# Performance work log

Measured on AMD Instinct MI355X. Metric: run time of the kernel, lower is better.

The kernel has to match this reference:

```python
import jax, jax.numpy as jnp
import numpy as np

B, IN, H = 131072, 128, 128


def _linear_params(key, out_dim, in_dim):
    k1, k2 = jax.random.split(key)
    bound = 1.0 / np.sqrt(in_dim)
    W = jax.random.uniform(k1, (out_dim, in_dim), jnp.float32, -bound, bound)
    b = jax.random.uniform(k2, (out_dim,), jnp.float32, -bound, bound)
    return W, b


def setup_inputs() -> dict:
    key = jax.random.key(0)
    ks = jax.random.split(key, 11)
    X = jax.random.normal(ks[0], (B, IN), jnp.float32)
    h_prev = jax.random.normal(ks[1], (B, H), jnp.float32)
    c_prev = jax.random.normal(ks[2], (B, H), jnp.float32)
    names = ['xf', 'hf', 'xi', 'hi', 'xc', 'hc', 'xo', 'ho']
    params = {}
    for i, n in enumerate(names):
        in_dim = IN if n[0] == 'x' else H
        W, b = _linear_params(ks[3 + i], H, in_dim)
        params[f'W_{n}'] = W
        params[f'b_{n}'] = b
    return {'X': X, 'h_prev': h_prev, 'c_prev': c_prev, **params}


def reference(X, h_prev, c_prev,
              W_xf, b_xf, W_hf, b_hf,
              W_xi, b_xi, W_hi, b_hi,
              W_xc, b_xc, W_hc, b_hc,
              W_xo, b_xo, W_ho, b_ho):
    # Fuse the 8 small GEMMs into 2 concatenated GEMMs (x->4H, h->4H)
    Wx = jnp.concatenate([W_xf, W_xi, W_xc, W_xo], axis=0)  # [4H, IN]
    Wh = jnp.concatenate([W_hf, W_hi, W_hc, W_ho], axis=0)  # [4H, H]
    bx = jnp.concatenate([b_xf, b_xi, b_xc, b_xo])
    bh = jnp.concatenate([b_hf, b_hi, b_hc, b_ho])
    gates = X @ Wx.T + h_prev @ Wh.T + bx + bh  # [B, 4H]
    f, i, c_til, o = jnp.split(gates, 4, axis=-1)
    f_t = jax.nn.sigmoid(f)
    i_t = jax.nn.sigmoid(i)
    c_tilde_t = jnp.tanh(c_til)
    o_t = jax.nn.sigmoid(o)
    c_t = f_t * c_prev + i_t * c_tilde_t
    h_t = o_t * jnp.tanh(c_t)
    return (h_t, c_t)
```

## Files before the change

kernel.cpp:

```cpp
#include <hip/hip_runtime.h>
#include <hip/hip_bf16.h>

#define B_ROWS 131072
#define H 128
#define SLAB 16
#define NSLAB 16
#define NBLK 512

typedef __bf16 bf16x8 __attribute__((ext_vector_type(8)));
typedef float f32x4 __attribute__((ext_vector_type(4)));

#define LOG2E 1.4426950408889634f

__device__ __forceinline__ float fast_sigmoid(float v) {
    return __builtin_amdgcn_rcpf(1.0f + __builtin_amdgcn_exp2f(-LOG2E * v));
}
__device__ __forceinline__ float fast_tanh(float v) {
    return 1.0f - 2.0f * __builtin_amdgcn_rcpf(1.0f + __builtin_amdgcn_exp2f(2.0f * LOG2E * v));
}

struct WPtrs {
    const float* wx[4];
    const float* wh[4];
    const float* bx[4];
    const float* bh[4];
};

__global__ __launch_bounds__(256) void prep_weights(WPtrs p, __bf16* __restrict__ wcat,
                                                    float* __restrict__ bsum) {
    int n = blockIdx.x;
    int k = threadIdx.x;
    int g = n >> 7, r = n & 127;
    float v = (k < H) ? p.wx[g][r * H + k] : p.wh[g][r * H + (k - H)];
    wcat[n * 256 + k] = (__bf16)v;
    if (k == 0) bsum[n] = p.bx[g][r] + p.bh[g][r];
}

__global__ __launch_bounds__(512, 1) void lstm_fused(
    const float* __restrict__ X, const float* __restrict__ Hp, const float* __restrict__ Cp,
    const __bf16* __restrict__ Wcat, const float* __restrict__ Bsum,
    float* __restrict__ out)
{
    __shared__ char abuf[2][SLAB * 512];

    const int t = threadIdx.x;
    const int lane = t & 63;
    const int wv = t >> 6;
    const int l16 = lane & 15;
    const int kg = lane >> 4;
    const long base = (long)blockIdx.x * (SLAB * NSLAB);
    const long c_off = (long)B_ROWS * H;
    const int j = wv * 16 + l16;

    bf16x8 wreg[4][8];
    {
        const __bf16* wb = Wcat + (long)j * 256 + kg * 8;
#pragma unroll
        for (int g = 0; g < 4; ++g)
#pragma unroll
            for (int kc = 0; kc < 8; ++kc) {
                wreg[g][kc] = *(const bf16x8*)(wb + g * (128 * 256) + kc * 32);
                asm volatile("" : "+v"(wreg[g][kc]));
            }
    }
    float bias[4];
#pragma unroll
    for (int g = 0; g < 4; ++g) bias[g] = Bsum[g * H + j];

    const int s_r = t >> 5;
    const int s_g8 = t & 31;

    auto stage_load = [&](float4* L, long srow) {
        const float* sp = (s_g8 < 16) ? (X + (srow + s_r) * H + s_g8 * 8)
                                      : (Hp + (srow + s_r) * H + (s_g8 - 16) * 8);
        L[0] = *(const float4*)sp;
        L[1] = *(const float4*)(sp + 4);
    };
    auto write_slab = [&](char* buf, const float4* W) {
        union { __bf16 e[8]; bf16x8 v; } u;
        float4 lo = W[0], hi = W[1];
        u.e[0] = (__bf16)lo.x; u.e[1] = (__bf16)lo.y;
        u.e[2] = (__bf16)lo.z; u.e[3] = (__bf16)lo.w;
        u.e[4] = (__bf16)hi.x; u.e[5] = (__bf16)hi.y;
        u.e[6] = (__bf16)hi.z; u.e[7] = (__bf16)hi.w;
        *(bf16x8*)(buf + s_r * 512 + ((s_g8 ^ (s_r & 7)) << 4)) = u.v;
    };
    auto load_cp = [&](float* c, long srow) {
#pragma unroll
        for (int r = 0; r < 4; ++r) c[r] = Cp[(srow + kg * 4 + r) * H + j];
    };

    float4 RA[2], RB[2];
    float cpv[4], cpn[4];

    stage_load(RB, base);
    load_cp(cpv, base);
    stage_load(RA, base + SLAB);
    write_slab(abuf[0], RB);

#define BODY(S, W, L, BW, BC) {                                                   \
    const long srow = base + (long)(S) * SLAB;                                    \
    const long pn1 = ((S) + 1 < NSLAB) ? (S) + 1 : NSLAB - 1;                     \
    const long pn2 = ((S) + 2 < NSLAB) ? (S) + 2 : NSLAB - 1;                     \
    stage_load(L, base + pn2 * SLAB);                                             \
    load_cp(cpn, base + pn1 * SLAB);                                              \
    asm volatile("s_waitcnt lgkmcnt(0)\n\ts_barrier" ::: "memory");               \
    write_slab(abuf[BW], W);                                                      \
    const char* ac = abuf[BC];                                                    \
    f32x4 acc[4] = {};                                                            \
    _Pragma("unroll")                                                             \
    for (int kc = 0; kc < 8; ++kc) {                                              \
        int slot = ((kc * 4 + kg) ^ (l16 & 7)) << 4;                              \
        bf16x8 av = *(const bf16x8*)(ac + l16 * 512 + slot);                      \
        _Pragma("unroll")                                                         \
        for (int g = 0; g < 4; ++g)                                               \
            acc[g] = __builtin_amdgcn_mfma_f32_16x16x32_bf16(av, wreg[g][kc], acc[g], 0, 0, 0); \
    }                                                                             \
    _Pragma("unroll")                                                             \
    for (int r = 0; r < 4; ++r) {                                                 \
        long row = srow + kg * 4 + r;                                             \
        float fg = acc[0][r] + bias[0];                                           \
        float ig = acc[1][r] + bias[1];                                           \
        float cg = acc[2][r] + bias[2];                                           \
        float og = acc[3][r] + bias[3];                                           \
        float ft = fast_sigmoid(fg);                                              \
        float it = fast_sigmoid(ig);                                              \
        float cc = fast_tanh(cg);                                                 \
        float ot = fast_sigmoid(og);                                              \
        float ct = ft * cpv[r] + it * cc;                                         \
        float ht = ot * fast_tanh(ct);                                            \
        out[row * H + j] = ht;                                                    \
        out[c_off + row * H + j] = ct;                                            \
    }                                                                             \
    _Pragma("unroll")                                                             \
    for (int r = 0; r < 4; ++r) cpv[r] = cpn[r];                                  \
}

    for (int sp = 0; sp < NSLAB / 2; ++sp) {
        BODY(2 * sp,     RA, RB, 1, 0);
        BODY(2 * sp + 1, RB, RA, 0, 1);
    }
#undef BODY
}

extern "C" void kernel_launch(void* const* d_in, const int* in_sizes, int n_in,
                              void* d_out, int out_size, void* d_ws, size_t ws_size,
                              hipStream_t stream) {
    const float* X  = (const float*)d_in[0];
    const float* Hp = (const float*)d_in[1];
    const float* Cp = (const float*)d_in[2];
    WPtrs p;
    p.wx[0] = (const float*)d_in[3];  p.bx[0] = (const float*)d_in[4];
    p.wh[0] = (const float*)d_in[5];  p.bh[0] = (const float*)d_in[6];
    p.wx[1] = (const float*)d_in[7];  p.bx[1] = (const float*)d_in[8];
    p.wh[1] = (const float*)d_in[9];  p.bh[1] = (const float*)d_in[10];
    p.wx[2] = (const float*)d_in[11]; p.bx[2] = (const float*)d_in[12];
    p.wh[2] = (const float*)d_in[13]; p.bh[2] = (const float*)d_in[14];
    p.wx[3] = (const float*)d_in[15]; p.bx[3] = (const float*)d_in[16];
    p.wh[3] = (const float*)d_in[17]; p.bh[3] = (const float*)d_in[18];

    __bf16* wcat = (__bf16*)d_ws;
    float*  bsum = (float*)((char*)d_ws + 512 * 256 * 2);

    prep_weights<<<512, 256, 0, stream>>>(p, wcat, bsum);
    lstm_fused<<<NBLK, 512, 0, stream>>>(X, Hp, Cp, wcat, bsum, (float*)d_out);
}
```

Baseline: 95.24 us.

## Swap MFMA operands for vectorized epilogue and stream weights from global

Slabs grow from 16 to 32 rows, and the MFMA operand roles are swapped so each lane's accumulator holds four consecutive hidden units of one row. This lets the c_prev loads and the h/c stores become 16-byte vector accesses instead of scalar ones strided by H. The 128 bf16 weight VGPRs are no longer held in registers; weights are reloaded from global memory (L2/L1) inside every MFMA loop. The aim is to cut memory transaction count in a bandwidth-bound kernel, at the cost of repeated weight loads in the inner loop.

```diff
diff --git a/kernel.cpp b/kernel.cpp
--- a/kernel.cpp
+++ b/kernel.cpp
@@ -3,8 +3,8 @@
 
 #define B_ROWS 131072
 #define H 128
-#define SLAB 16
-#define NSLAB 16
+#define SLAB 32
+#define NSLAB 8
 #define NBLK 512
 
 typedef __bf16 bf16x8 __attribute__((ext_vector_type(8)));
@@ -46,52 +46,58 @@
     const int t = threadIdx.x;
     const int lane = t & 63;
     const int wv = t >> 6;
+    const int rg = wv >> 2;
+    const int ug = wv & 3;
     const int l16 = lane & 15;
     const int kg = lane >> 4;
     const long base = (long)blockIdx.x * (SLAB * NSLAB);
     const long c_off = (long)B_ROWS * H;
-    const int j = wv * 16 + l16;
 
-    bf16x8 wreg[4][8];
-    {
-        const __bf16* wb = Wcat + (long)j * 256 + kg * 8;
+    const __bf16* wbase = Wcat + ((long)(ug * 32 + l16)) * 256 + kg * 8;
+    const int ubase = ug * 32 + kg * 4;
+
+    f32x4 bias4[4][2];
 #pragma unroll
-        for (int g = 0; g < 4; ++g)
+    for (int g = 0; g < 4; ++g)
 #pragma unroll
-            for (int kc = 0; kc < 8; ++kc) {
-                wreg[g][kc] = *(const bf16x8*)(wb + g * (128 * 256) + kc * 32);
-                asm volatile("" : "+v"(wreg[g][kc]));
-            }
-    }
-    float bias[4];
-#pragma unroll
-    for (int g = 0; g < 4; ++g) bias[g] = Bsum[g * H + j];
+        for (int ut = 0; ut < 2; ++ut)
+            bias4[g][ut] = *(const f32x4*)(Bsum + g * H + ubase + ut * 16);
 
     const int s_r = t >> 5;
     const int s_g8 = t & 31;
 
     auto stage_load = [&](float4* L, long srow) {
-        const float* sp = (s_g8 < 16) ? (X + (srow + s_r) * H + s_g8 * 8)
-                                      : (Hp + (srow + s_r) * H + (s_g8 - 16) * 8);
-        L[0] = *(const float4*)sp;
-        L[1] = *(const float4*)(sp + 4);
+#pragma unroll
+        for (int q = 0; q < 2; ++q) {
+            int row = q * 16 + s_r;
+            const float* sp = (s_g8 < 16) ? (X + (srow + row) * H + s_g8 * 8)
+                                          : (Hp + (srow + row) * H + (s_g8 - 16) * 8);
+            L[q * 2]     = *(const float4*)sp;
+            L[q * 2 + 1] = *(const float4*)(sp + 4);
+        }
     };
     auto write_slab = [&](char* buf, const float4* W) {
-        union { __bf16 e[8]; bf16x8 v; } u;
-        float4 lo = W[0], hi = W[1];
-        u.e[0] = (__bf16)lo.x; u.e[1] = (__bf16)lo.y;
-        u.e[2] = (__bf16)lo.z; u.e[3] = (__bf16)lo.w;
-        u.e[4] = (__bf16)hi.x; u.e[5] = (__bf16)hi.y;
-        u.e[6] = (__bf16)hi.z; u.e[7] = (__bf16)hi.w;
-        *(bf16x8*)(buf + s_r * 512 + ((s_g8 ^ (s_r & 7)) << 4)) = u.v;
+#pragma unroll
+        for (int q = 0; q < 2; ++q) {
+            int row = q * 16 + s_r;
+            union { __bf16 e[8]; bf16x8 v; } u;
+            float4 lo = W[q * 2], hi = W[q * 2 + 1];
+            u.e[0] = (__bf16)lo.x; u.e[1] = (__bf16)lo.y;
+            u.e[2] = (__bf16)lo.z; u.e[3] = (__bf16)lo.w;
+            u.e[4] = (__bf16)hi.x; u.e[5] = (__bf16)hi.y;
+            u.e[6] = (__bf16)hi.z; u.e[7] = (__bf16)hi.w;
+            *(bf16x8*)(buf + row * 512 + ((s_g8 ^ (row & 7)) << 4)) = u.v;
+        }
     };
-    auto load_cp = [&](float* c, long srow) {
+    auto load_cp = [&](f32x4* c, long srow) {
+        const float* cb = Cp + (srow + rg * 16 + l16) * (long)H + ubase;
 #pragma unroll
-        for (int r = 0; r < 4; ++r) c[r] = Cp[(srow + kg * 4 + r) * H + j];
+        for (int ut = 0; ut < 2; ++ut)
+            c[ut] = *(const f32x4*)(cb + ut * 16);
     };
 
-    float4 RA[2], RB[2];
-    float cpv[4], cpn[4];
+    float4 RA[4], RB[4];
+    f32x4 cpv[2], cpn[2];
 
     stage_load(RB, base);
     load_cp(cpv, base);
@@ -107,33 +113,43 @@
     asm volatile("s_waitcnt lgkmcnt(0)\n\ts_barrier" ::: "memory");               \
     write_slab(abuf[BW], W);                                                      \
     const char* ac = abuf[BC];                                                    \
-    f32x4 acc[4] = {};                                                            \
+    f32x4 acc[4][2] = {};                                                         \
+    const int arow = rg * 16 + l16;                                               \
     _Pragma("unroll")                                                             \
     for (int kc = 0; kc < 8; ++kc) {                                              \
-        int slot = ((kc * 4 + kg) ^ (l16 & 7)) << 4;                              \
-        bf16x8 av = *(const bf16x8*)(ac + l16 * 512 + slot);                      \
+        bf16x8 xf = *(const bf16x8*)(ac + arow * 512 + (((kc * 4 + kg) ^ (arow & 7)) << 4)); \
         _Pragma("unroll")                                                         \
-        for (int g = 0; g < 4; ++g)                                               \
-            acc[g] = __builtin_amdgcn_mfma_f32_16x16x32_bf16(av, wreg[g][kc], acc[g], 0, 0, 0); \
+        for (int g = 0; g < 4; ++g) {                                             \
+            _Pragma("unroll")                                                     \
+            for (int ut = 0; ut < 2; ++ut) {                                      \
+                bf16x8 wf = *(const bf16x8*)(wbase + (g * 128 + ut * 16) * 256 + kc * 32); \
+                acc[g][ut] = __builtin_amdgcn_mfma_f32_16x16x32_bf16(wf, xf, acc[g][ut], 0, 0, 0); \
+            }                                                                     \
+        }                                                                         \
     }                                                                             \
+    const long brow = srow + rg * 16 + l16;                                       \
     _Pragma("unroll")                                                             \
-    for (int r = 0; r < 4; ++r) {                                                 \
-        long row = srow + kg * 4 + r;                                             \
-        float fg = acc[0][r] + bias[0];                                           \
-        float ig = acc[1][r] + bias[1];                                           \
-        float cg = acc[2][r] + bias[2];                                           \
-        float og = acc[3][r] + bias[3];                                           \
-        float ft = fast_sigmoid(fg);                                              \
-        float it = fast_sigmoid(ig);                                              \
-        float cc = fast_tanh(cg);                                                 \
-        float ot = fast_sigmoid(og);                                              \
-        float ct = ft * cpv[r] + it * cc;                                         \
-        float ht = ot * fast_tanh(ct);                                            \
-        out[row * H + j] = ht;                                                    \
-        out[c_off + row * H + j] = ct;                                            \
+    for (int ut = 0; ut < 2; ++ut) {                                              \
+        f32x4 hv, cv;                                                             \
+        _Pragma("unroll")                                                         \
+        for (int r = 0; r < 4; ++r) {                                             \
+            float fg = acc[0][ut][r] + bias4[0][ut][r];                           \
+            float ig = acc[1][ut][r] + bias4[1][ut][r];                           \
+            float cg = acc[2][ut][r] + bias4[2][ut][r];                           \
+            float og = acc[3][ut][r] + bias4[3][ut][r];                           \
+            float ft = fast_sigmoid(fg);                                          \
+            float it = fast_sigmoid(ig);                                          \
+            float cc = fast_tanh(cg);                                             \
+            float ot = fast_sigmoid(og);                                          \
+            float ct = ft * cpv[ut][r] + it * cc;                                 \
+            float ht = ot * fast_tanh(ct);                                        \
+            hv[r] = ht;                                                           \
+            cv[r] = ct;                                                           \
+        }                                                                         \
+        *(f32x4*)(out + brow * H + ubase + ut * 16) = hv;                         \
+        *(f32x4*)(out + c_off + brow * H + ubase + ut * 16) = cv;                 \
     }                                                                             \
-    _Pragma("unroll")                                                             \
-    for (int r = 0; r < 4; ++r) cpv[r] = cpn[r];                                  \
+    cpv[0] = cpn[0]; cpv[1] = cpn[1];                                             \
 }
 
     for (int sp = 0; sp < NSLAB / 2; ++sp) {
```

After: 292.0 us. 207% more time.

## Split hidden units across blocks with interleaved gate weights to raise occupancy

Applied to the files above, without the earlier changes.

Weights are reordered so each hidden unit's four gates are adjacent. Each 256-thread block now handles a quarter of the hidden units over its row range, so every wave holds only two gate tiles in registers instead of four, which lets three blocks share a CU. Lane pairs exchange gate values with shuffles, and each lane of a pair computes the cell update but stores only one of h or c. The cost is that each block re-reads the same X/h_prev rows four times (one per hidden-unit quarter), and the c_prev prefetch is dropped, so it is now loaded inside the slab loop with less latency hiding.

```diff
diff --git a/kernel.cpp b/kernel.cpp
--- a/kernel.cpp
+++ b/kernel.cpp
@@ -5,7 +5,7 @@
 #define H 128
 #define SLAB 16
 #define NSLAB 16
-#define NBLK 512
+#define NBLK 2048
 
 typedef __bf16 bf16x8 __attribute__((ext_vector_type(8)));
 typedef float f32x4 __attribute__((ext_vector_type(4)));
@@ -28,17 +28,17 @@
 
 __global__ __launch_bounds__(256) void prep_weights(WPtrs p, __bf16* __restrict__ wcat,
                                                     float* __restrict__ bsum) {
-    int n = blockIdx.x;
+    int n2 = blockIdx.x;
     int k = threadIdx.x;
-    int g = n >> 7, r = n & 127;
-    float v = (k < H) ? p.wx[g][r * H + k] : p.wh[g][r * H + (k - H)];
-    wcat[n * 256 + k] = (__bf16)v;
-    if (k == 0) bsum[n] = p.bx[g][r] + p.bh[g][r];
+    int g = n2 & 3, u = n2 >> 2;
+    float v = (k < H) ? p.wx[g][u * H + k] : p.wh[g][u * H + (k - H)];
+    wcat[n2 * 256 + k] = (__bf16)v;
+    if (k == 0) bsum[n2] = p.bx[g][u] + p.bh[g][u];
 }
 
-__global__ __launch_bounds__(512, 1) void lstm_fused(
+__global__ __launch_bounds__(256, 3) void lstm_fused(
     const float* __restrict__ X, const float* __restrict__ Hp, const float* __restrict__ Cp,
-    const __bf16* __restrict__ Wcat, const float* __restrict__ Bsum,
+    const __bf16* __restrict__ Wcat2, const float* __restrict__ Bsum,
     float* __restrict__ out)
 {
     __shared__ char abuf[2][SLAB * 512];
@@ -48,92 +48,103 @@
     const int wv = t >> 6;
     const int l16 = lane & 15;
     const int kg = lane >> 4;
-    const long base = (long)blockIdx.x * (SLAB * NSLAB);
+    const int Bk = blockIdx.x;
+    const int uq = (Bk >> 3) & 3;
+    const int rb = (Bk & 7) | ((Bk >> 5) << 3);
+    const long base = (long)rb * (SLAB * NSLAB);
     const long c_off = (long)B_ROWS * H;
-    const int j = wv * 16 + l16;
+    const int unit = uq * 32 + wv * 8 + (l16 >> 1);
+    const int gp = l16 & 1;
 
-    bf16x8 wreg[4][8];
-    {
-        const __bf16* wb = Wcat + (long)j * 256 + kg * 8;
+    bf16x8 wreg[2][8];
 #pragma unroll
-        for (int g = 0; g < 4; ++g)
+    for (int t2 = 0; t2 < 2; ++t2) {
+        const __bf16* wb = Wcat2 + ((long)(unit * 4 + 2 * t2 + gp)) * 256 + kg * 8;
 #pragma unroll
-            for (int kc = 0; kc < 8; ++kc) {
-                wreg[g][kc] = *(const bf16x8*)(wb + g * (128 * 256) + kc * 32);
-                asm volatile("" : "+v"(wreg[g][kc]));
-            }
+        for (int kc = 0; kc < 8; ++kc) {
+            wreg[t2][kc] = *(const bf16x8*)(wb + kc * 32);
+            asm volatile("" : "+v"(wreg[t2][kc]));
+        }
     }
-    float bias[4];
+    float bias2[2];
 #pragma unroll
-    for (int g = 0; g < 4; ++g) bias[g] = Bsum[g * H + j];
+    for (int t2 = 0; t2 < 2; ++t2) bias2[t2] = Bsum[unit * 4 + 2 * t2 + gp];
 
-    const int s_r = t >> 5;
-    const int s_g8 = t & 31;
+    const int s_r = t >> 4;
+    const int s_c = t & 15;
 
     auto stage_load = [&](float4* L, long srow) {
-        const float* sp = (s_g8 < 16) ? (X + (srow + s_r) * H + s_g8 * 8)
-                                      : (Hp + (srow + s_r) * H + (s_g8 - 16) * 8);
+        const float* sp = (s_c < 8) ? (X + (srow + s_r) * H + s_c * 16)
+                                    : (Hp + (srow + s_r) * H + (s_c - 8) * 16);
         L[0] = *(const float4*)sp;
         L[1] = *(const float4*)(sp + 4);
+        L[2] = *(const float4*)(sp + 8);
+        L[3] = *(const float4*)(sp + 12);
     };
     auto write_slab = [&](char* buf, const float4* W) {
-        union { __bf16 e[8]; bf16x8 v; } u;
-        float4 lo = W[0], hi = W[1];
-        u.e[0] = (__bf16)lo.x; u.e[1] = (__bf16)lo.y;
-        u.e[2] = (__bf16)lo.z; u.e[3] = (__bf16)lo.w;
-        u.e[4] = (__bf16)hi.x; u.e[5] = (__bf16)hi.y;
-        u.e[6] = (__bf16)hi.z; u.e[7] = (__bf16)hi.w;
-        *(bf16x8*)(buf + s_r * 512 + ((s_g8 ^ (s_r & 7)) << 4)) = u.v;
-    };
-    auto load_cp = [&](float* c, long srow) {
 #pragma unroll
-        for (int r = 0; r < 4; ++r) c[r] = Cp[(srow + kg * 4 + r) * H + j];
+        for (int hh = 0; hh < 2; ++hh) {
+            union { __bf16 e[8]; bf16x8 v; } u;
+            float4 lo = W[hh * 2], hi = W[hh * 2 + 1];
+            u.e[0] = (__bf16)lo.x; u.e[1] = (__bf16)lo.y;
+            u.e[2] = (__bf16)lo.z; u.e[3] = (__bf16)lo.w;
+            u.e[4] = (__bf16)hi.x; u.e[5] = (__bf16)hi.y;
+            u.e[6] = (__bf16)hi.z; u.e[7] = (__bf16)hi.w;
+            int sl = s_c * 2 + hh;
+            *(bf16x8*)(buf + s_r * 512 + ((sl ^ (s_r & 7)) << 4)) = u.v;
+        }
     };
 
-    float4 RA[2], RB[2];
-    float cpv[4], cpn[4];
+    float4 RA[4], RB[4];
+    float cpv[4];
 
     stage_load(RB, base);
-    load_cp(cpv, base);
+    write_slab(abuf[0], RB);
     stage_load(RA, base + SLAB);
-    write_slab(abuf[0], RB);
 
 #define BODY(S, W, L, BW, BC) {                                                   \
     const long srow = base + (long)(S) * SLAB;                                    \
-    const long pn1 = ((S) + 1 < NSLAB) ? (S) + 1 : NSLAB - 1;                     \
+    _Pragma("unroll")                                                             \
+    for (int r = 0; r < 4; ++r)                                                   \
+        cpv[r] = Cp[(srow + kg * 4 + r) * (long)H + unit];                        \
     const long pn2 = ((S) + 2 < NSLAB) ? (S) + 2 : NSLAB - 1;                     \
     stage_load(L, base + pn2 * SLAB);                                             \
-    load_cp(cpn, base + pn1 * SLAB);                                              \
     asm volatile("s_waitcnt lgkmcnt(0)\n\ts_barrier" ::: "memory");               \
     write_slab(abuf[BW], W);                                                      \
     const char* ac = abuf[BC];                                                    \
-    f32x4 acc[4] = {};                                                            \
+    f32x4 acc[2] = {};                                                            \
     _Pragma("unroll")                                                             \
     for (int kc = 0; kc < 8; ++kc) {                                              \
         int slot = ((kc * 4 + kg) ^ (l16 & 7)) << 4;                              \
         bf16x8 av = *(const bf16x8*)(ac + l16 * 512 + slot);                      \
-        _Pragma("unroll")                                                         \
-        for (int g = 0; g < 4; ++g)                                               \
-            acc[g] = __builtin_amdgcn_mfma_f32_16x16x32_bf16(av, wreg[g][kc], acc[g], 0, 0, 0); \
+        acc[0] = __builtin_amdgcn_mfma_f32_16x16x32_bf16(av, wreg[0][kc], acc[0], 0, 0, 0); \
+        acc[1] = __builtin_amdgcn_mfma_f32_16x16x32_bf16(av, wreg[1][kc], acc[1], 0, 0, 0); \
     }                                                                             \
     _Pragma("unroll")                                                             \
+    for (int r = 0; r < 4; ++r) { acc[0][r] += bias2[0]; acc[1][r] += bias2[1]; } \
+    f32x4 sh0, sh1;                                                               \
+    _Pragma("unroll")                                                             \
     for (int r = 0; r < 4; ++r) {                                                 \
-        long row = srow + kg * 4 + r;                                             \
-        float fg = acc[0][r] + bias[0];                                           \
-        float ig = acc[1][r] + bias[1];                                           \
-        float cg = acc[2][r] + bias[2];                                           \
-        float og = acc[3][r] + bias[3];                                           \
+        sh0[r] = __shfl_xor(acc[0][r], 1);                                        \
+        sh1[r] = __shfl_xor(acc[1][r], 1);                                        \
+    }                                                                             \
+    const bool oddl = lane & 1;                                                   \
+    _Pragma("unroll")                                                             \
+    for (int r = 0; r < 4; ++r) {                                                 \
+        float fg = oddl ? sh0[r] : acc[0][r];                                     \
+        float ig = oddl ? acc[0][r] : sh0[r];                                     \
+        float cg = oddl ? sh1[r] : acc[1][r];                                     \
+        float og = oddl ? acc[1][r] : sh1[r];                                     \
         float ft = fast_sigmoid(fg);                                              \
         float it = fast_sigmoid(ig);                                              \
         float cc = fast_tanh(cg);                                                 \
         float ot = fast_sigmoid(og);                                              \
         float ct = ft * cpv[r] + it * cc;                                         \
         float ht = ot * fast_tanh(ct);                                            \
-        out[row * H + j] = ht;                                                    \
-        out[c_off + row * H + j] = ct;                                            \
+        long row = srow + kg * 4 + r;                                             \
+        float* dst = oddl ? (out + c_off + row * H + unit) : (out + row * H + unit); \
+        *dst = oddl ? ct : ht;                                                    \
     }                                                                             \
-    _Pragma("unroll")                                                             \
-    for (int r = 0; r < 4; ++r) cpv[r] = cpn[r];                                  \
 }
 
     for (int sp = 0; sp < NSLAB / 2; ++sp) {
@@ -163,5 +174,5 @@
     float*  bsum = (float*)((char*)d_ws + 512 * 256 * 2);
 
     prep_weights<<<512, 256, 0, stream>>>(p, wcat, bsum);
-    lstm_fused<<<NBLK, 512, 0, stream>>>(X, Hp, Cp, wcat, bsum, (float*)d_out);
+    lstm_fused<<<NBLK, 256, 0, stream>>>(X, Hp, Cp, wcat, bsum, (float*)d_out);
 }
```

New measurement: 134.7 us. +41.4%, slower.
